# Performance work log

Hardware: AMD Instinct MI355X
Metric: run time of the kernel (lower is better)

Reference implementation:

```python
import jax, jax.numpy as jnp
import numpy as np


def setup_inputs() -> dict:
    key = jax.random.key(0)
    B, N, C = 16, 4096, 768  # SAM ViT-B token tensor [batch, tokens, channels]
    x = jax.random.normal(key, (B, N, C), dtype=jnp.float32)
    k = 384        # int(C * p2) with p2 = 0.5
    largest = 1    # torch.topk largest=True
    return {"x": x, "k": k, "largest": largest}


def reference(x, k, largest):
    # torch.topk(x, k, dim=2, largest=largest) with dim=2 == last axis for 3D x,
    # then scatter values back into zeros_like(x) at the selected indices.
    if largest:
        vals, idx = jax.lax.top_k(x, k)            # [B, N, k]
    else:
        neg_vals, idx = jax.lax.top_k(-x, k)
        vals = -neg_vals
    B, N, _ = x.shape
    b = jnp.arange(B)[:, None, None]               # broadcast batch index
    n = jnp.arange(N)[None, :, None]               # broadcast token index
    out = jnp.zeros_like(x).at[b, n, idx].set(vals)
    return out
```

## Files before the change

### kernel.cpp

```cpp
#include <hip/hip_runtime.h>
#include <cstdint>


constexpr int C   = 768;
constexpr int TPB = 256;
constexpr int WPB = TPB / 64;
constexpr int EPL = C / 64;
constexpr int NV  = EPL / 4;

__device__ __forceinline__ uint32_t f2key(uint32_t b, uint32_t flip) {
    uint32_t m = (uint32_t)((int32_t)b >> 31) | 0x80000000u;
    return (b ^ m) ^ flip;
}
__device__ __forceinline__ float key2f(uint32_t key, uint32_t flip) {
    uint32_t u = key ^ flip;
    uint32_t m = (~(uint32_t)((int32_t)u >> 31)) | 0x80000000u;
    return __uint_as_float(u ^ m);
}

__global__ __launch_bounds__(TPB, 8) void topk_scatter_row(
        const float* __restrict__ x,
        const int*   __restrict__ pk,
        const int*   __restrict__ plg,
        float*       __restrict__ out,
        int rows) {
    const int lane = threadIdx.x & 63;
    const int wid  = threadIdx.x >> 6;
    const int row  = blockIdx.x * WPB + wid;
    if (row >= rows) return;

    const float* xr   = x   + (size_t)row * C;
    float*       orow = out + (size_t)row * C;

    const int      k    = pk[0];
    const uint32_t flip = (plg[0] != 0) ? 0u : 0xFFFFFFFFu;

    uint32_t key[EPL];
    #pragma unroll
    for (int j = 0; j < NV; ++j) {
        uint4 t = ((const uint4*)xr)[j * 64 + lane];
        key[j*4+0] = f2key(t.x, flip);
        key[j*4+1] = f2key(t.y, flip);
        key[j*4+2] = f2key(t.z, flip);
        key[j*4+3] = f2key(t.w, flip);
    }

    if (k <= 0) {
        #pragma unroll
        for (int j = 0; j < NV; ++j)
            ((float4*)orow)[j * 64 + lane] = make_float4(0.f, 0.f, 0.f, 0.f);
        return;
    }
    if (k >= C) {
        #pragma unroll
        for (int j = 0; j < NV; ++j) {
            float4 o; float* oo = (float*)&o;
            #pragma unroll
            for (int c2 = 0; c2 < 4; ++c2) oo[c2] = key2f(key[j*4+c2], flip);
            ((float4*)orow)[j * 64 + lane] = o;
        }
        return;
    }

    uint32_t T = 0;
    bool exact = false;
    for (int b = 31; b >= 0; --b) {
        const uint32_t cand = T | (1u << b);
        int cnt = 0;
        #pragma unroll
        for (int e = 0; e < EPL; ++e)
            cnt += __popcll(__ballot(key[e] >= cand));
        if (cnt >= k) {
            T = cand;
            if (cnt == k) { exact = true; break; }
        }
    }

    uint32_t selmask = 0;
    if (exact) {
        #pragma unroll
        for (int e = 0; e < EPL; ++e)
            if (key[e] >= T) selmask |= 1u << e;
    } else {
        int cgt = 0;
        #pragma unroll
        for (int e = 0; e < EPL; ++e) {
            if (key[e] > T) selmask |= 1u << e;
            cgt += __popcll(__ballot(key[e] > T));
        }
        const int need = k - cgt;
        const unsigned long long below = (1ull << lane) - 1ull;
        int base = 0;
        #pragma unroll
        for (int j = 0; j < NV; ++j) {
            int eq[4]; unsigned long long m[4];
            #pragma unroll
            for (int c2 = 0; c2 < 4; ++c2) {
                eq[c2] = (key[j*4+c2] == T) ? 1 : 0;
                m[c2]  = __ballot(eq[c2] != 0);
            }
            int lanebelow = 0;
            #pragma unroll
            for (int c2 = 0; c2 < 4; ++c2) lanebelow += __popcll(m[c2] & below);
            int own = 0;
            #pragma unroll
            for (int c2 = 0; c2 < 4; ++c2) {
                if (eq[c2] && (base + lanebelow + own) < need)
                    selmask |= 1u << (j*4 + c2);
                own += eq[c2];
            }
            #pragma unroll
            for (int c2 = 0; c2 < 4; ++c2) base += __popcll(m[c2]);
        }
    }

    #pragma unroll
    for (int j = 0; j < NV; ++j) {
        float4 o; float* oo = (float*)&o;
        #pragma unroll
        for (int c2 = 0; c2 < 4; ++c2) {
            const int e = j*4 + c2;
            oo[c2] = ((selmask >> e) & 1u) ? key2f(key[e], flip) : 0.0f;
        }
        ((float4*)orow)[j * 64 + lane] = o;
    }
}

extern "C" void kernel_launch(void* const* d_in, const int* in_sizes, int n_in,
                              void* d_out, int out_size, void* d_ws, size_t ws_size,
                              hipStream_t stream) {
    const float* x   = (const float*)d_in[0];
    const int*   pk  = (const int*)d_in[1];
    const int*   plg = (const int*)d_in[2];
    float*       out = (float*)d_out;

    const int rows   = in_sizes[0] / C;
    const int blocks = (rows + WPB - 1) / WPB;
    topk_scatter_row<<<blocks, TPB, 0, stream>>>(x, pk, plg, out, rows);
}
```

Before: 333.3 us.

## Process multiple rows per wavefront with prefetch of next row and nontemporal memory ops

Each wavefront now handles 8 consecutive rows instead of one and loads the next row into registers while it runs the radix-select on the current row, so global-load latency overlaps with the ballot-heavy compute. Loads and stores now use nontemporal builtins to avoid polluting cache with streamed data. The cost is 8x fewer blocks (2048 for 65536 rows), which may hurt latency hiding through occupancy, plus extra register pressure from the prefetch buffer.

```diff
diff --git a/kernel.cpp b/kernel.cpp
--- a/kernel.cpp
+++ b/kernel.cpp
@@ -7,6 +7,10 @@
 constexpr int WPB = TPB / 64;
 constexpr int EPL = C / 64;
 constexpr int NV  = EPL / 4;
+constexpr int RPW = 8;
+
+typedef uint32_t uint4v  __attribute__((ext_vector_type(4)));
+typedef float    float4v __attribute__((ext_vector_type(4)));
 
 __device__ __forceinline__ uint32_t f2key(uint32_t b, uint32_t flip) {
     uint32_t m = (uint32_t)((int32_t)b >> 31) | 0x80000000u;
@@ -26,103 +30,117 @@
         int rows) {
     const int lane = threadIdx.x & 63;
     const int wid  = threadIdx.x >> 6;
-    const int row  = blockIdx.x * WPB + wid;
-    if (row >= rows) return;
-
-    const float* xr   = x   + (size_t)row * C;
-    float*       orow = out + (size_t)row * C;
+    const int row0 = (blockIdx.x * WPB + wid) * RPW;
+    if (row0 >= rows) return;
 
     const int      k    = pk[0];
     const uint32_t flip = (plg[0] != 0) ? 0u : 0xFFFFFFFFu;
 
-    uint32_t key[EPL];
+    const uint4v* xv = (const uint4v*)(x + (size_t)row0 * C);
+    const int nrow = (rows - row0 < RPW) ? (rows - row0) : RPW;
+
+    uint4v pre[NV];
     #pragma unroll
-    for (int j = 0; j < NV; ++j) {
-        uint4 t = ((const uint4*)xr)[j * 64 + lane];
-        key[j*4+0] = f2key(t.x, flip);
-        key[j*4+1] = f2key(t.y, flip);
-        key[j*4+2] = f2key(t.z, flip);
-        key[j*4+3] = f2key(t.w, flip);
-    }
+    for (int j = 0; j < NV; ++j)
+        pre[j] = __builtin_nontemporal_load(&xv[j * 64 + lane]);
 
-    if (k <= 0) {
-        #pragma unroll
-        for (int j = 0; j < NV; ++j)
-            ((float4*)orow)[j * 64 + lane] = make_float4(0.f, 0.f, 0.f, 0.f);
-        return;
-    }
-    if (k >= C) {
+    for (int i = 0; i < nrow; ++i) {
+        uint32_t key[EPL];
         #pragma unroll
         for (int j = 0; j < NV; ++j) {
-            float4 o; float* oo = (float*)&o;
             #pragma unroll
-            for (int c2 = 0; c2 < 4; ++c2) oo[c2] = key2f(key[j*4+c2], flip);
-            ((float4*)orow)[j * 64 + lane] = o;
+            for (int c2 = 0; c2 < 4; ++c2)
+                key[j*4+c2] = f2key(pre[j][c2], flip);
         }
-        return;
-    }
+        if (i + 1 < nrow) {
+            const uint4v* xn = xv + (size_t)(i + 1) * (C / 4);
+            #pragma unroll
+            for (int j = 0; j < NV; ++j)
+                pre[j] = __builtin_nontemporal_load(&xn[j * 64 + lane]);
+        }
 
-    uint32_t T = 0;
-    bool exact = false;
-    for (int b = 31; b >= 0; --b) {
-        const uint32_t cand = T | (1u << b);
-        int cnt = 0;
-        #pragma unroll
-        for (int e = 0; e < EPL; ++e)
-            cnt += __popcll(__ballot(key[e] >= cand));
-        if (cnt >= k) {
-            T = cand;
-            if (cnt == k) { exact = true; break; }
+        float4v* orow = (float4v*)(out + (size_t)(row0 + i) * C);
+
+        if (k <= 0) {
+            const float4v z = {0.f, 0.f, 0.f, 0.f};
+            #pragma unroll
+            for (int j = 0; j < NV; ++j)
+                __builtin_nontemporal_store(z, &orow[j * 64 + lane]);
+            continue;
         }
-    }
+        if (k >= C) {
+            #pragma unroll
+            for (int j = 0; j < NV; ++j) {
+                float4v o;
+                #pragma unroll
+                for (int c2 = 0; c2 < 4; ++c2) o[c2] = key2f(key[j*4+c2], flip);
+                __builtin_nontemporal_store(o, &orow[j * 64 + lane]);
+            }
+            continue;
+        }
 
-    uint32_t selmask = 0;
-    if (exact) {
-        #pragma unroll
-        for (int e = 0; e < EPL; ++e)
-            if (key[e] >= T) selmask |= 1u << e;
-    } else {
-        int cgt = 0;
-        #pragma unroll
-        for (int e = 0; e < EPL; ++e) {
-            if (key[e] > T) selmask |= 1u << e;
-            cgt += __popcll(__ballot(key[e] > T));
+        uint32_t T = 0;
+        bool exact = false;
+        for (int b = 31; b >= 0; --b) {
+            const uint32_t cand = T | (1u << b);
+            int cnt = 0;
+            #pragma unroll
+            for (int e = 0; e < EPL; ++e)
+                cnt += __popcll(__ballot(key[e] >= cand));
+            if (cnt >= k) {
+                T = cand;
+                if (cnt == k) { exact = true; break; }
+            }
         }
-        const int need = k - cgt;
-        const unsigned long long below = (1ull << lane) - 1ull;
-        int base = 0;
+
+        uint32_t selmask = 0;
+        if (exact) {
+            #pragma unroll
+            for (int e = 0; e < EPL; ++e)
+                if (key[e] >= T) selmask |= 1u << e;
+        } else {
+            int cgt = 0;
+            #pragma unroll
+            for (int e = 0; e < EPL; ++e) {
+                if (key[e] > T) selmask |= 1u << e;
+                cgt += __popcll(__ballot(key[e] > T));
+            }
+            const int need = k - cgt;
+            const unsigned long long below = (1ull << lane) - 1ull;
+            int base = 0;
+            #pragma unroll
+            for (int j = 0; j < NV; ++j) {
+                int eq[4]; unsigned long long m[4];
+                #pragma unroll
+                for (int c2 = 0; c2 < 4; ++c2) {
+                    eq[c2] = (key[j*4+c2] == T) ? 1 : 0;
+                    m[c2]  = __ballot(eq[c2] != 0);
+                }
+                int lanebelow = 0;
+                #pragma unroll
+                for (int c2 = 0; c2 < 4; ++c2) lanebelow += __popcll(m[c2] & below);
+                int own = 0;
+                #pragma unroll
+                for (int c2 = 0; c2 < 4; ++c2) {
+                    if (eq[c2] && (base + lanebelow + own) < need)
+                        selmask |= 1u << (j*4 + c2);
+                    own += eq[c2];
+                }
+                #pragma unroll
+                for (int c2 = 0; c2 < 4; ++c2) base += __popcll(m[c2]);
+            }
+        }
+
         #pragma unroll
         for (int j = 0; j < NV; ++j) {
-            int eq[4]; unsigned long long m[4];
+            float4v o;
             #pragma unroll
             for (int c2 = 0; c2 < 4; ++c2) {
-                eq[c2] = (key[j*4+c2] == T) ? 1 : 0;
-                m[c2]  = __ballot(eq[c2] != 0);
+                const int e = j*4 + c2;
+                o[c2] = ((selmask >> e) & 1u) ? key2f(key[e], flip) : 0.0f;
             }
-            int lanebelow = 0;
-            #pragma unroll
-            for (int c2 = 0; c2 < 4; ++c2) lanebelow += __popcll(m[c2] & below);
-            int own = 0;
-            #pragma unroll
-            for (int c2 = 0; c2 < 4; ++c2) {
-                if (eq[c2] && (base + lanebelow + own) < need)
-                    selmask |= 1u << (j*4 + c2);
-                own += eq[c2];
-            }
-            #pragma unroll
-            for (int c2 = 0; c2 < 4; ++c2) base += __popcll(m[c2]);
+            __builtin_nontemporal_store(o, &orow[j * 64 + lane]);
         }
-    }
-
-    #pragma unroll
-    for (int j = 0; j < NV; ++j) {
-        float4 o; float* oo = (float*)&o;
-        #pragma unroll
-        for (int c2 = 0; c2 < 4; ++c2) {
-            const int e = j*4 + c2;
-            oo[c2] = ((selmask >> e) & 1u) ? key2f(key[e], flip) : 0.0f;
-        }
-        ((float4*)orow)[j * 64 + lane] = o;
     }
 }
 
@@ -134,7 +152,8 @@
     const int*   plg = (const int*)d_in[2];
     float*       out = (float*)d_out;
 
-    const int rows   = in_sizes[0] / C;
-    const int blocks = (rows + WPB - 1) / WPB;
+    const int rows      = in_sizes[0] / C;
+    const int rows_blk  = WPB * RPW;
+    const int blocks    = (rows + rows_blk - 1) / rows_blk;
     topk_scatter_row<<<blocks, TPB, 0, stream>>>(x, pk, plg, out, rows);
 }
```

Result: slower. 346.6 us (+4.0%).
